# Kernel optimization log

Measured on AMD Instinct MI355X. Metric: run time of the kernel, lower is better.

## Reference

```python
import jax, jax.numpy as jnp
import numpy as np
from jax import lax

B, C, H, W = 2048, 3, 64, 64
NUM_NODES = 20
N = B * NUM_NODES


def _edges():
    # fully-connected (no self loop) 20-node graph, replicated per batch element
    i, j = np.meshgrid(np.arange(NUM_NODES), np.arange(NUM_NODES), indexing='ij')
    m = i != j
    src, dst = i[m], j[m]  # 380 edges per graph
    off = (np.arange(B) * NUM_NODES)[:, None]
    rows = (src[None] + off).reshape(-1)
    cols = (dst[None] + off).reshape(-1)
    return jnp.asarray(np.stack([rows, cols]), dtype=jnp.int32)  # [2, B*380]


def setup_inputs() -> dict:
    key = jax.random.key(0)
    ks = jax.random.split(key, 8)
    return dict(
        im=jax.random.uniform(ks[0], (B, C, H, W), jnp.float32),
        x=jax.random.normal(ks[1], (N, 2), jnp.float32),
        edge_index=_edges(),
        conv1_w=jax.random.normal(ks[2], (10, 3, 11, 11), jnp.float32) * 0.05,
        conv2_w=jax.random.normal(ks[3], (16, 10, 5, 5), jnp.float32) * 0.05,
        conv2_b=jnp.zeros((16,), jnp.float32),
        lin_w=jax.random.normal(ks[4], (2, 64), jnp.float32) * 0.1,
        lin_b=jnp.zeros((2,), jnp.float32),
        g1_w=jax.random.normal(ks[5], (8, 4), jnp.float32) * 0.3,
        g1_b=jnp.zeros((8,), jnp.float32),
        g2_w=jax.random.normal(ks[6], (1, 8), jnp.float32) * 0.3,
        g2_b=jnp.zeros((1,), jnp.float32),
    )


def _maxpool(h, k, s):
    return lax.reduce_window(h, -jnp.inf, lax.max, (1, 1, k, k), (1, 1, s, s), 'VALID')


def _gcn(x, edge_index, Wt, b, improved, aggr):
    # PyG GCNConv: linear (no bias) -> gcn_norm with self-loops -> scatter aggr -> +bias
    x = x @ Wt.T
    n = x.shape[0]
    fill = 2.0 if improved else 1.0  # improved adds self-loop weight 2
    loop = jnp.arange(n, dtype=edge_index.dtype)
    row = jnp.concatenate([edge_index[0], loop])  # source (flow=source_to_target)
    col = jnp.concatenate([edge_index[1], loop])  # target
    ew = jnp.concatenate([jnp.ones(edge_index.shape[1], x.dtype), jnp.full((n,), fill, x.dtype)])
    deg = jax.ops.segment_sum(ew, col, num_segments=n)
    dis = jnp.where(deg > 0, lax.rsqrt(jnp.maximum(deg, 1e-12)), 0.0)
    norm = dis[row] * ew * dis[col]
    msg = norm[:, None] * x[row]  # gather + weight
    if aggr == 'mean':
        s = jax.ops.segment_sum(msg, col, num_segments=n)
        cnt = jax.ops.segment_sum(jnp.ones_like(norm), col, num_segments=n)
        out = s / jnp.maximum(cnt, 1.0)[:, None]
    else:  # max
        out = jax.ops.segment_max(msg, col, num_segments=n)
        out = jnp.where(jnp.isfinite(out), out, 0.0)
    return out + b


def reference(im, x, edge_index, conv1_w, conv2_w, conv2_b, lin_w, lin_b, g1_w, g1_b, g2_w, g2_b):
    dn = ('NCHW', 'OIHW', 'NCHW')
    h = lax.conv_general_dilated(im, conv1_w, (4, 4), [(2, 2), (2, 2)], dimension_numbers=dn)
    h = jax.nn.leaky_relu(h)          # slope 0.01, matches nn.LeakyReLU default
    h = _maxpool(h, 3, 2)             # [B,10,7,7]
    h = lax.conv_general_dilated(h, conv2_w, (2, 2), [(2, 2), (2, 2)], dimension_numbers=dn)
    h = h + conv2_b[None, :, None, None]
    h = jax.nn.leaky_relu(h)
    h = _maxpool(h, 2, 2)             # [B,16,2,2]
    h = h.reshape(-1, 64)
    img_feat = jax.nn.sigmoid(h @ lin_w.T + lin_b)  # [B,2]
    xin = jnp.concatenate([x, jnp.repeat(img_feat, NUM_NODES, axis=0)], axis=1)  # [N,4]
    h1 = jax.nn.leaky_relu(_gcn(xin, edge_index, g1_w, g1_b, False, 'mean'))
    h2 = _gcn(h1, edge_index, g2_w, g2_b, True, 'max')  # [N,1]
    out = jax.nn.softmax(h2.reshape(B, NUM_NODES), axis=1)
    return out, img_feat
```

## Files before the change

kernel.cpp:

```cpp
#include <hip/hip_runtime.h>
#include <hip/hip_bf16.h>
#include <math.h>


#define PLW 72
#define PLANE_SH (PLW * 68)
#define PLANE_B (PLANE_SH * 2)
#define IMG_B (PLANE_B + 4848)
#define SMEM_BYTES (4 * IMG_B)

#define MEMBAR() asm volatile("" ::: "memory")

typedef __attribute__((ext_vector_type(8))) short bf16x8;
typedef __attribute__((ext_vector_type(4))) float f32x4;

__device__ inline unsigned short f2bf(float f) {
    unsigned u = __float_as_uint(f);
    u += 0x7fff + ((u >> 16) & 1);
    return (unsigned short)(u >> 16);
}

__global__ void reorder_weights(const float* __restrict__ w1,
                                const float* __restrict__ w2,
                                unsigned char* __restrict__ ws) {
    unsigned short* bN = (unsigned short*)ws;
    unsigned short* bS = (unsigned short*)(ws + 18432);
    float* w2t = (float*)(ws + 36864);
    const int id = blockIdx.x * 256 + threadIdx.x;
    for (int e = id; e < 9216; e += 4096) {
        int j = e & 7, lane = (e >> 3) & 63, s = e >> 9;
        int n = lane & 15, q = lane >> 4;
        int c = s / 6, kyp = s - c * 6;
        int k = q * 8 + j;
        int ky = 2 * kyp + (k >> 4);
        int kxN = k & 15, kxS = (k & 15) - 4;
        unsigned short vN = 0, vS = 0;
        if (n < 10 && ky < 11) {
            const float* wr = w1 + n * 363 + c * 121 + ky * 11;
            if (kxN < 11) vN = f2bf(wr[kxN]);
            if (kxS >= 0 && kxS < 11) vS = f2bf(wr[kxS]);
        }
        bN[e] = vN;
        bS[e] = vS;
    }
    for (int i = id; i < 4000; i += 4096) {
        int k = i & 15, tap = i >> 4;
        w2t[i] = w2[k * 250 + tap];
    }
}

__global__ __launch_bounds__(256, 2) void cnn_mfma(
        const float* __restrict__ im,
        const unsigned char* __restrict__ wsb,
        const float* __restrict__ conv2_b,
        const float* __restrict__ lin_w,
        const float* __restrict__ lin_b,
        float* __restrict__ out) {
    __shared__ __align__(16) unsigned char smem[SMEM_BYTES];
    const int t = threadIdx.x, lane = t & 63, wid = t >> 6;
    const int img = blockIdx.x * 4 + wid;
    const int n = lane & 15, q = lane >> 4;

    unsigned char* base = smem + wid * IMG_B;
    unsigned short* plane = (unsigned short*)base;
    float* out1 = (float*)base;
    float* p1pf = (float*)(base + PLANE_B);
    float* out2f = p1pf;

    if (lane < 20) out[img * 20 + lane] = 0.05f;

    for (int i = lane; i < 264; i += 64) {
        if (i < 72) {
            int rr = i / 18, cu = i - rr * 18;
            int r = (rr < 2) ? rr : (64 + rr);
            *((unsigned long long*)(plane + r * PLW) + cu) = 0ull;
        } else {
            int s2 = i - 72;
            int r = 2 + s2 / 3, j = s2 - (s2 / 3) * 3;
            unsigned short* row = plane + r * PLW;
            if (j == 0)      *(unsigned int*)(row) = 0u;
            else if (j == 1) *(unsigned int*)(row + 66) = 0u;
            else             *(unsigned long long*)(row + 68) = 0ull;
        }
    }
    MEMBAR();

    const int lofs = (q >> 1) * 72 + (q & 1) * 8;
    int eb[15];
#pragma unroll
    for (int T = 0; T < 15; ++T) {
        const bool even = T < 8;
        int idx = even ? T : T - 8;
        int i = idx * 16 + n;
        int oy, cb;
        if (even) {
            oy = min(i >> 3, 14);
            cb = (i & 7) << 3;
        } else {
            int oyu = i / 7, rem = i - oyu * 7;
            oy = min(oyu, 14);
            cb = rem << 3;
        }
        eb[T] = 288 * oy + cb + lofs;
    }

    f32x4 acc[15];
#pragma unroll
    for (int i = 0; i < 15; ++i) acc[i] = (f32x4)(0.0f);

    const unsigned short* bNl = (const unsigned short*)wsb + lane * 8;
    const unsigned short* bSl = (const unsigned short*)(wsb + 18432) + lane * 8;

    const float4* imc = (const float4*)(im + (size_t)img * 12288);
    float4 pf[16];
#pragma unroll
    for (int it = 0; it < 16; ++it) pf[it] = imc[it * 64 + lane];

    for (int c = 0; c < 3; ++c) {
#pragma unroll
        for (int it = 0; it < 16; ++it) {
            int idx = it * 64 + lane;
            int y = idx >> 4, x4 = (idx & 15) << 2;
            int e = (y + 2) * PLW + x4 + 2;
            *(__hip_bfloat162*)(&plane[e]) =
                __float22bfloat162_rn(make_float2(pf[it].x, pf[it].y));
            *(__hip_bfloat162*)(&plane[e + 2]) =
                __float22bfloat162_rn(make_float2(pf[it].z, pf[it].w));
        }
        MEMBAR();
        if (c < 2) {
            const float4* imcn = imc + (c + 1) * 1024;
#pragma unroll
            for (int it = 0; it < 16; ++it) pf[it] = imcn[it * 64 + lane];
        }
#pragma unroll 1
        for (int kyp = 0; kyp < 6; ++kyp) {
            const int s = c * 6 + kyp;
            bf16x8 bfE = *(const bf16x8*)(bNl + s * 512);
            bf16x8 bfO = *(const bf16x8*)(bSl + s * 512);
            const int ro = kyp * 144;
#pragma unroll
            for (int T = 0; T < 15; ++T) {
                bf16x8 a = *(const bf16x8*)(&plane[eb[T] + ro]);
                acc[T] = __builtin_amdgcn_mfma_f32_16x16x32_bf16(
                    a, (T < 8) ? bfE : bfO, acc[T], 0, 0, 0);
            }
        }
        MEMBAR();
    }

#pragma unroll
    for (int T = 0; T < 15; ++T) {
        const bool even = T < 8;
        int idx = even ? T : T - 8;
#pragma unroll
        for (int r = 0; r < 4; ++r) {
            int i = idx * 16 + (q << 2) + r;
            float v = acc[T][r];
            v = v > 0.0f ? v : 0.01f * v;
            if (n < 10) {
                if (even) {
                    if (i < 120) out1[n * 225 + (i >> 3) * 15 + ((i & 7) << 1)] = v;
                } else {
                    if (i < 105) {
                        int oyu = i / 7;
                        out1[n * 225 + oyu * 15 + (i - oyu * 7) * 2 + 1] = v;
                    }
                }
            }
        }
    }
    MEMBAR();

    for (int i = lane; i < 490; i += 64) {
        int c2 = i / 49, rr = (i % 49) / 7, col = i % 7;
        const float* o1 = &out1[c2 * 225 + (2 * rr) * 15 + 2 * col];
        float m = o1[0];
        m = fmaxf(m, o1[1]);  m = fmaxf(m, o1[2]);
        m = fmaxf(m, o1[15]); m = fmaxf(m, o1[16]); m = fmaxf(m, o1[17]);
        m = fmaxf(m, o1[30]); m = fmaxf(m, o1[31]); m = fmaxf(m, o1[32]);
        p1pf[c2 * 121 + (rr + 2) * 11 + (col + 2)] = m;
    }
    for (int i = lane; i < 720; i += 64) {
        int c2 = i / 72, r = i - c2 * 72;
        int row, col;
        if (r < 44) {
            int rr = r / 11;
            row = (rr < 2) ? rr : 7 + rr;
            col = r - rr * 11;
        } else {
            int r2 = r - 44;
            row = 2 + (r2 >> 2);
            int cc = r2 & 3;
            col = (cc < 2) ? cc : 7 + cc;
        }
        p1pf[c2 * 121 + row * 11 + col] = 0.0f;
    }
    MEMBAR();

    {
        const float* w2t = (const float*)(wsb + 36864);
        const int pix2 = lane >> 2, kg = lane & 3;
        const int o2y = pix2 >> 2, o2x = pix2 & 3;
        float ax = 0.f, ay = 0.f, az = 0.f, aw = 0.f;
#pragma unroll 1
        for (int c2 = 0; c2 < 10; ++c2) {
#pragma unroll
            for (int ky = 0; ky < 5; ++ky) {
#pragma unroll
                for (int kx = 0; kx < 5; ++kx) {
                    float v = p1pf[c2 * 121 + (o2y * 2 + ky) * 11 + o2x * 2 + kx];
                    float4 w = *(const float4*)(w2t + (c2 * 25 + ky * 5 + kx) * 16 + kg * 4);
                    ax = fmaf(v, w.x, ax); ay = fmaf(v, w.y, ay);
                    az = fmaf(v, w.z, az); aw = fmaf(v, w.w, aw);
                }
            }
        }
        MEMBAR();
        float4 r;
        r.x = ax + conv2_b[kg * 4 + 0];
        r.y = ay + conv2_b[kg * 4 + 1];
        r.z = az + conv2_b[kg * 4 + 2];
        r.w = aw + conv2_b[kg * 4 + 3];
        r.x = r.x > 0.0f ? r.x : 0.01f * r.x;
        r.y = r.y > 0.0f ? r.y : 0.01f * r.y;
        r.z = r.z > 0.0f ? r.z : 0.01f * r.z;
        r.w = r.w > 0.0f ? r.w : 0.01f * r.w;
        *(float4*)(&out2f[pix2 * 16 + kg * 4]) = r;
    }
    MEMBAR();

    {
        const int k = lane >> 2, qy = (lane >> 1) & 1, qx = lane & 1;
        const int p0 = (2 * qy) * 4 + 2 * qx;
        float hb = fmaxf(fmaxf(out2f[p0 * 16 + k], out2f[(p0 + 1) * 16 + k]),
                         fmaxf(out2f[(p0 + 4) * 16 + k], out2f[(p0 + 5) * 16 + k]));
        float pa = hb * lin_w[lane];
        float pb = hb * lin_w[64 + lane];
#pragma unroll
        for (int m = 32; m >= 1; m >>= 1) {
            pa += __shfl_xor(pa, m);
            pb += __shfl_xor(pb, m);
        }
        if (lane == 0) {
            out[40960 + img * 2 + 0] = 1.0f / (1.0f + expf(-(pa + lin_b[0])));
            out[40960 + img * 2 + 1] = 1.0f / (1.0f + expf(-(pb + lin_b[1])));
        }
    }
}

__global__ __launch_bounds__(256) void cnn_fallback(
        const float* __restrict__ im, const float* __restrict__ w1,
        const float* __restrict__ w2, const float* __restrict__ conv2_b,
        const float* __restrict__ lin_w, const float* __restrict__ lin_b,
        float* __restrict__ out) {
    __shared__ __align__(16) float bufA[68 * 68];
    const int b = blockIdx.x, t = threadIdx.x;
    if (t < 20) out[b * 20 + t] = 0.05f;
    for (int i = t; i < 68 * 68; i += 256) bufA[i] = 0.0f;
    float acc[10];
#pragma unroll
    for (int i = 0; i < 10; ++i) acc[i] = 0.0f;
    const int oy = min(t / 15, 14), ox = t % 15;
    for (int c = 0; c < 3; ++c) {
        __syncthreads();
        const float4* imc = (const float4*)(im + ((size_t)(b * 3 + c)) * 4096);
        for (int i = t; i < 1024; i += 256) {
            float4 v = imc[i];
            int y = i >> 4, x4 = (i & 15) << 2;
            float* dst = &bufA[(y + 2) * 68 + x4 + 2];
            dst[0] = v.x; dst[1] = v.y; dst[2] = v.z; dst[3] = v.w;
        }
        __syncthreads();
#pragma unroll 1
        for (int ky = 0; ky < 11; ++ky) {
            const float* row = &bufA[(oy * 4 + ky) * 68 + ox * 4];
            float4 r0 = *(const float4*)(row);
            float4 r1 = *(const float4*)(row + 4);
            float4 r2 = *(const float4*)(row + 8);
            float in[12] = {r0.x, r0.y, r0.z, r0.w, r1.x, r1.y, r1.z, r1.w,
                            r2.x, r2.y, r2.z, r2.w};
#pragma unroll
            for (int kx = 0; kx < 11; ++kx) {
                float v = in[kx];
#pragma unroll
                for (int oc = 0; oc < 10; ++oc)
                    acc[oc] = fmaf(v, w1[oc * 363 + c * 121 + ky * 11 + kx], acc[oc]);
            }
        }
    }
    __syncthreads();
    if (t < 225) {
#pragma unroll
        for (int oc = 0; oc < 10; ++oc) {
            float v = acc[oc];
            bufA[oc * 225 + t] = v > 0.0f ? v : 0.01f * v;
        }
    }
    float* p1p = bufA + 3100;
    for (int i = t; i < 1210; i += 256) p1p[i] = 0.0f;
    __syncthreads();
    for (int i = t; i < 490; i += 256) {
        int c2 = i / 49, r = (i % 49) / 7, col = i % 7;
        const float* o1 = &bufA[c2 * 225 + (2 * r) * 15 + 2 * col];
        float m = o1[0];
        m = fmaxf(m, o1[1]);  m = fmaxf(m, o1[2]);
        m = fmaxf(m, o1[15]); m = fmaxf(m, o1[16]); m = fmaxf(m, o1[17]);
        m = fmaxf(m, o1[30]); m = fmaxf(m, o1[31]); m = fmaxf(m, o1[32]);
        p1p[c2 * 121 + (r + 2) * 11 + (col + 2)] = m;
    }
    __syncthreads();
    float* out2 = bufA;
    float* hbuf = bufA + 256;
    {
        const int k = t & 15, pix = t >> 4;
        const int o2y = pix >> 2, o2x = pix & 3;
        float a2 = 0.0f;
#pragma unroll 1
        for (int c2 = 0; c2 < 10; ++c2)
#pragma unroll
            for (int ky = 0; ky < 5; ++ky)
#pragma unroll
                for (int kx = 0; kx < 5; ++kx) {
                    float v = p1p[c2 * 121 + (o2y * 2 + ky) * 11 + o2x * 2 + kx];
                    a2 = fmaf(v, w2[k * 250 + c2 * 25 + ky * 5 + kx], a2);
                }
        a2 += conv2_b[k];
        a2 = a2 > 0.0f ? a2 : 0.01f * a2;
        __syncthreads();
        out2[k * 16 + pix] = a2;
    }
    __syncthreads();
    if (t < 64) {
        int k = t >> 2, qy = (t >> 1) & 1, qx = t & 1;
        const float* o2 = &out2[k * 16 + (2 * qy) * 4 + 2 * qx];
        hbuf[t] = fmaxf(fmaxf(o2[0], o2[1]), fmaxf(o2[4], o2[5]));
    }
    __syncthreads();
    if (t < 128) {
        int o = t >> 6, l = t & 63;
        float p = hbuf[l] * lin_w[o * 64 + l];
#pragma unroll
        for (int m = 32; m >= 1; m >>= 1) p += __shfl_xor(p, m);
        if (l == 0)
            out[40960 + b * 2 + o] = 1.0f / (1.0f + expf(-(p + lin_b[o])));
    }
}

extern "C" void kernel_launch(void* const* d_in, const int* in_sizes, int n_in,
                              void* d_out, int out_size, void* d_ws, size_t ws_size,
                              hipStream_t stream) {
    const float* im = (const float*)d_in[0];
    const float* w1 = (const float*)d_in[3];
    const float* w2 = (const float*)d_in[4];
    const float* b2 = (const float*)d_in[5];
    const float* lw = (const float*)d_in[6];
    const float* lb = (const float*)d_in[7];
    float* out = (float*)d_out;

    if (ws_size >= 52864) {
        reorder_weights<<<16, 256, 0, stream>>>(w1, w2, (unsigned char*)d_ws);
        cnn_mfma<<<512, 256, 0, stream>>>(im, (const unsigned char*)d_ws,
                                          b2, lw, lb, out);
    } else {
        cnn_fallback<<<2048, 256, 0, stream>>>(im, w1, w2, b2, lw, lb, out);
    }
}
```

Before: 193.5 us.

## Prefetch MFMA weights, batch LDS A-loads, pad scratch strides for vector loads

The next kernel-row's bf16 weight fragments are now loaded one iteration ahead, and all 15 A operands are loaded before the MFMA chain is issued. This hides global and LDS latency behind the matrix ops. The image channel is now loaded right before its conversion instead of being prefetched across the MFMA loop, which lowers register pressure but gives up that overlap. The out1 and p1pf scratch buffers get padded strides so the maxpool and conv2 stages can use float2 loads, and zeroing of the p1pf border moves to the kernel prologue.

```diff
diff --git a/kernel.cpp b/kernel.cpp
--- a/kernel.cpp
+++ b/kernel.cpp
@@ -6,7 +6,9 @@
 #define PLW 72
 #define PLANE_SH (PLW * 68)
 #define PLANE_B (PLANE_SH * 2)
-#define IMG_B (PLANE_B + 4848)
+#define OUT1_STR 240
+#define P1P_STR 132
+#define IMG_B (PLANE_B + 1320 * 4)
 #define SMEM_BYTES (4 * IMG_B)
 
 #define MEMBAR() asm volatile("" ::: "memory")
@@ -83,6 +85,21 @@
             else             *(unsigned long long*)(row + 68) = 0ull;
         }
     }
+    for (int i = lane; i < 720; i += 64) {
+        int c2 = i / 72, r = i - c2 * 72;
+        int row, col;
+        if (r < 44) {
+            int rr = r / 11;
+            row = (rr < 2) ? rr : 7 + rr;
+            col = r - rr * 11;
+        } else {
+            int r2 = r - 44;
+            row = 2 + (r2 >> 2);
+            int cc = r2 & 3;
+            col = (cc < 2) ? cc : 7 + cc;
+        }
+        p1pf[c2 * P1P_STR + row * 12 + col] = 0.0f;
+    }
     MEMBAR();
 
     const int lofs = (q >> 1) * 72 + (q & 1) * 8;
@@ -110,41 +127,48 @@
 
     const unsigned short* bNl = (const unsigned short*)wsb + lane * 8;
     const unsigned short* bSl = (const unsigned short*)(wsb + 18432) + lane * 8;
-
     const float4* imc = (const float4*)(im + (size_t)img * 12288);
-    float4 pf[16];
-#pragma unroll
-    for (int it = 0; it < 16; ++it) pf[it] = imc[it * 64 + lane];
+
+    bf16x8 bfE = *(const bf16x8*)(bNl);
+    bf16x8 bfO = *(const bf16x8*)(bSl);
 
     for (int c = 0; c < 3; ++c) {
-#pragma unroll
-        for (int it = 0; it < 16; ++it) {
-            int idx = it * 64 + lane;
-            int y = idx >> 4, x4 = (idx & 15) << 2;
-            int e = (y + 2) * PLW + x4 + 2;
-            *(__hip_bfloat162*)(&plane[e]) =
-                __float22bfloat162_rn(make_float2(pf[it].x, pf[it].y));
-            *(__hip_bfloat162*)(&plane[e + 2]) =
-                __float22bfloat162_rn(make_float2(pf[it].z, pf[it].w));
+        {
+            const float4* imcc = imc + c * 1024;
+            float4 v[16];
+#pragma unroll
+            for (int it = 0; it < 16; ++it) v[it] = imcc[it * 64 + lane];
+#pragma unroll
+            for (int it = 0; it < 16; ++it) {
+                int idx = it * 64 + lane;
+                int y = idx >> 4, x4 = (idx & 15) << 2;
+                int e = (y + 2) * PLW + x4 + 2;
+                *(__hip_bfloat162*)(&plane[e]) =
+                    __float22bfloat162_rn(make_float2(v[it].x, v[it].y));
+                *(__hip_bfloat162*)(&plane[e + 2]) =
+                    __float22bfloat162_rn(make_float2(v[it].z, v[it].w));
+            }
         }
         MEMBAR();
-        if (c < 2) {
-            const float4* imcn = imc + (c + 1) * 1024;
-#pragma unroll
-            for (int it = 0; it < 16; ++it) pf[it] = imcn[it * 64 + lane];
-        }
 #pragma unroll 1
         for (int kyp = 0; kyp < 6; ++kyp) {
             const int s = c * 6 + kyp;
-            bf16x8 bfE = *(const bf16x8*)(bNl + s * 512);
-            bf16x8 bfO = *(const bf16x8*)(bSl + s * 512);
+            bf16x8 nE = bfE, nO = bfO;
+            if (s < 17) {
+                nE = *(const bf16x8*)(bNl + (s + 1) * 512);
+                nO = *(const bf16x8*)(bSl + (s + 1) * 512);
+            }
             const int ro = kyp * 144;
-#pragma unroll
-            for (int T = 0; T < 15; ++T) {
-                bf16x8 a = *(const bf16x8*)(&plane[eb[T] + ro]);
+            bf16x8 a[15];
+#pragma unroll
+            for (int T = 0; T < 15; ++T)
+                a[T] = *(const bf16x8*)(&plane[eb[T] + ro]);
+#pragma unroll
+            for (int T = 0; T < 15; ++T)
                 acc[T] = __builtin_amdgcn_mfma_f32_16x16x32_bf16(
-                    a, (T < 8) ? bfE : bfO, acc[T], 0, 0, 0);
-            }
+                    a[T], (T < 8) ? bfE : bfO, acc[T], 0, 0, 0);
+            bfE = nE;
+            bfO = nO;
         }
         MEMBAR();
     }
@@ -160,11 +184,12 @@
             v = v > 0.0f ? v : 0.01f * v;
             if (n < 10) {
                 if (even) {
-                    if (i < 120) out1[n * 225 + (i >> 3) * 15 + ((i & 7) << 1)] = v;
+                    if (i < 120)
+                        out1[n * OUT1_STR + (i >> 3) * 16 + ((i & 7) << 1)] = v;
                 } else {
                     if (i < 105) {
                         int oyu = i / 7;
-                        out1[n * 225 + oyu * 15 + (i - oyu * 7) * 2 + 1] = v;
+                        out1[n * OUT1_STR + oyu * 16 + (i - oyu * 7) * 2 + 1] = v;
                     }
                 }
             }
@@ -174,27 +199,14 @@
 
     for (int i = lane; i < 490; i += 64) {
         int c2 = i / 49, rr = (i % 49) / 7, col = i % 7;
-        const float* o1 = &out1[c2 * 225 + (2 * rr) * 15 + 2 * col];
-        float m = o1[0];
-        m = fmaxf(m, o1[1]);  m = fmaxf(m, o1[2]);
-        m = fmaxf(m, o1[15]); m = fmaxf(m, o1[16]); m = fmaxf(m, o1[17]);
-        m = fmaxf(m, o1[30]); m = fmaxf(m, o1[31]); m = fmaxf(m, o1[32]);
-        p1pf[c2 * 121 + (rr + 2) * 11 + (col + 2)] = m;
-    }
-    for (int i = lane; i < 720; i += 64) {
-        int c2 = i / 72, r = i - c2 * 72;
-        int row, col;
-        if (r < 44) {
-            int rr = r / 11;
-            row = (rr < 2) ? rr : 7 + rr;
-            col = r - rr * 11;
-        } else {
-            int r2 = r - 44;
-            row = 2 + (r2 >> 2);
-            int cc = r2 & 3;
-            col = (cc < 2) ? cc : 7 + cc;
-        }
-        p1pf[c2 * 121 + row * 11 + col] = 0.0f;
+        const float* o1 = &out1[c2 * OUT1_STR + (2 * rr) * 16 + 2 * col];
+        float2 r0 = *(const float2*)(o1);       float r0c = o1[2];
+        float2 r1 = *(const float2*)(o1 + 16);  float r1c = o1[18];
+        float2 r2 = *(const float2*)(o1 + 32);  float r2c = o1[34];
+        float m = fmaxf(fmaxf(r0.x, r0.y), r0c);
+        m = fmaxf(m, fmaxf(fmaxf(r1.x, r1.y), r1c));
+        m = fmaxf(m, fmaxf(fmaxf(r2.x, r2.y), r2c));
+        p1pf[c2 * P1P_STR + (rr + 2) * 12 + (col + 2)] = m;
     }
     MEMBAR();
 
@@ -205,14 +217,20 @@
         float ax = 0.f, ay = 0.f, az = 0.f, aw = 0.f;
 #pragma unroll 1
         for (int c2 = 0; c2 < 10; ++c2) {
+            const float* pc = &p1pf[c2 * P1P_STR + o2x * 2];
+            const float* wc = w2t + c2 * 400 + kg * 4;
 #pragma unroll
             for (int ky = 0; ky < 5; ++ky) {
+                const float* row = pc + (o2y * 2 + ky) * 12;
+                float2 A = *(const float2*)(row);
+                float2 B = *(const float2*)(row + 2);
+                float  C = row[4];
+                float vv[5] = {A.x, A.y, B.x, B.y, C};
 #pragma unroll
                 for (int kx = 0; kx < 5; ++kx) {
-                    float v = p1pf[c2 * 121 + (o2y * 2 + ky) * 11 + o2x * 2 + kx];
-                    float4 w = *(const float4*)(w2t + (c2 * 25 + ky * 5 + kx) * 16 + kg * 4);
-                    ax = fmaf(v, w.x, ax); ay = fmaf(v, w.y, ay);
-                    az = fmaf(v, w.z, az); aw = fmaf(v, w.w, aw);
+                    float4 w = *(const float4*)(wc + (ky * 5 + kx) * 16);
+                    ax = fmaf(vv[kx], w.x, ax); ay = fmaf(vv[kx], w.y, ay);
+                    az = fmaf(vv[kx], w.z, az); aw = fmaf(vv[kx], w.w, aw);
                 }
             }
         }
```

After: 192.3 us. Within noise of the previous version (-0.6%).
